# Optimization experiments

Hardware: AMD Instinct MI355X
Metric: run time of the kernel (lower is better)

The kernel has to match this reference:

```python
import jax, jax.numpy as jnp
import numpy as np

N, E, F_IN, EDGE_DIM, EMB, H, L, DENSE = 50000, 800000, 16, 4, 32, 4, 2, 128
HC = EMB * H


def setup_inputs() -> dict:
    ks = iter(jax.random.split(jax.random.key(0), 64))

    def w(shape, fan):
        return jax.random.normal(next(ks), shape, jnp.float32) / np.float32(np.sqrt(fan))

    inp = {}
    inp['x'] = jax.random.normal(next(ks), (N, F_IN), jnp.float32)
    inp['edge_index'] = jax.random.randint(next(ks), (2, E), 0, N, jnp.int32)
    inp['edge_attr'] = jax.random.normal(next(ks), (E, EDGE_DIM), jnp.float32)
    # layer-0 TransformerConv (F_IN -> EMB, H heads) + transf Linear
    inp['Wq0'] = w((F_IN, HC), F_IN); inp['bq0'] = w((HC,), HC)
    inp['Wk0'] = w((F_IN, HC), F_IN); inp['bk0'] = w((HC,), HC)
    inp['Wv0'] = w((F_IN, HC), F_IN); inp['bv0'] = w((HC,), HC)
    inp['We0'] = w((EDGE_DIM, HC), EDGE_DIM)
    inp['Ws0'] = w((F_IN, HC), F_IN); inp['bs0'] = w((HC,), HC)
    inp['Wt0'] = w((HC, EMB), HC); inp['bt0'] = w((EMB,), EMB)
    # stacked L inner layers (EMB -> EMB)
    inp['Wq'] = w((L, EMB, HC), EMB); inp['bq'] = w((L, HC), HC)
    inp['Wk'] = w((L, EMB, HC), EMB); inp['bk'] = w((L, HC), HC)
    inp['Wv'] = w((L, EMB, HC), EMB); inp['bv'] = w((L, HC), HC)
    inp['We'] = w((L, EDGE_DIM, HC), EDGE_DIM)
    inp['Ws'] = w((L, EMB, HC), EMB); inp['bs'] = w((L, HC), HC)
    inp['Wt'] = w((L, HC, EMB), HC); inp['bt'] = w((L, EMB), EMB)
    # dense head
    inp['W1'] = w((EMB, DENSE), EMB); inp['b1'] = w((DENSE,), DENSE)
    inp['W2'] = w((DENSE, DENSE // 2), DENSE); inp['b2'] = w((DENSE // 2,), DENSE)
    inp['W3'] = w((DENSE // 2, 1), DENSE // 2); inp['b3'] = w((1,), 1)
    return inp


def _tconv(h, edge_attr, src, dst, Wq, bq, Wk, bk, Wv, bv, We, Ws, bs):
    """PyG TransformerConv: edge-conditioned multi-head attention + root skip."""
    n = h.shape[0]
    q = (h @ Wq + bq).reshape(n, H, EMB)
    k = (h @ Wk + bk).reshape(n, H, EMB)
    v = (h @ Wv + bv).reshape(n, H, EMB)
    e = (edge_attr @ We).reshape(-1, H, EMB)          # [E,H,C]
    kj = k[src] + e                                   # gather + edge bias
    logits = (q[dst] * kj).sum(-1) / np.float32(np.sqrt(EMB))  # [E,H]
    m = jax.ops.segment_max(logits, dst, num_segments=n)       # segment softmax
    p = jnp.exp(logits - m[dst])
    z = jax.ops.segment_sum(p, dst, num_segments=n)
    alpha = p / (z[dst] + 1e-16)
    msg = (v[src] + e) * alpha[:, :, None]
    out = jax.ops.segment_sum(msg, dst, num_segments=n).reshape(n, HC)
    return out + h @ Ws + bs                          # root_weight skip


def _forward(x, edge_attr, Wq0, bq0, Wk0, bk0, Wv0, bv0, We0, Ws0, bs0, Wt0, bt0,
             Wq, bq, Wk, bk, Wv, bv, We, Ws, bs, Wt, bt,
             W1, b1, W2, b2, W3, b3, edge_index):
    src, dst = edge_index[0], edge_index[1]
    h = _tconv(x, edge_attr, src, dst, Wq0, bq0, Wk0, bk0, Wv0, bv0, We0, Ws0, bs0)
    h = jax.nn.relu(h @ Wt0 + bt0)
    for i in range(L):
        h = _tconv(h, edge_attr, src, dst, Wq[i], bq[i], Wk[i], bk[i],
                   Wv[i], bv[i], We[i], Ws[i], bs[i])
        h = jax.nn.relu(h @ Wt[i] + bt[i])
    h = jax.nn.relu(h @ W1 + b1)
    h = jax.nn.relu(h @ W2 + b2)
    return jax.nn.sigmoid(h @ W3 + b3)                # [N,1]


def reference(x, edge_index, edge_attr, Wq0, bq0, Wk0, bk0, Wv0, bv0, We0, Ws0, bs0,
              Wt0, bt0, Wq, bq, Wk, bk, Wv, bv, We, Ws, bs, Wt, bt,
              W1, b1, W2, b2, W3, b3):
    return _forward(x, edge_attr, Wq0, bq0, Wk0, bk0, Wv0, bv0, We0, Ws0, bs0,
                    Wt0, bt0, Wq, bq, Wk, bk, Wv, bv, We, Ws, bs, Wt, bt,
                    W1, b1, W2, b2, W3, b3, edge_index)
```

## Files before the change

### kernel.cpp

```cpp
#include <hip/hip_runtime.h>

#define NN 50000
#define EE 800000
#define FIN 16
#define EDIM 4
#define EMB 32
#define NH 4
#define HC 128
#define NL 2
#define DENSE 128
#define QNPB 50
#define SBLK 49

__device__ __forceinline__ float2 h2f2(unsigned int u) {
    union { unsigned int u; _Float16 h[2]; } c; c.u = u;
    return make_float2((float)c.h[0], (float)c.h[1]);
}
__device__ __forceinline__ unsigned int pkh2(float a, float b) {
    union { unsigned int u; _Float16 h[2]; } c;
    c.h[0] = (_Float16)a; c.h[1] = (_Float16)b; return c.u;
}

__global__ void hist_kernel(const int* __restrict__ dst, int* __restrict__ counts) {
    int e = blockIdx.x * blockDim.x + threadIdx.x;
    if (e < EE) atomicAdd(&counts[dst[e]], 1);
}

__global__ __launch_bounds__(1024) void scan1_kernel(const int* __restrict__ cursor,
                                                     int* __restrict__ row_ptr,
                                                     int* __restrict__ bsum) {
    __shared__ int wsum[16];
    __shared__ int wpre[17];
    int tid = threadIdx.x, lane = tid & 63, wid = tid >> 6;
    int i = blockIdx.x * 1024 + tid;
    int v = (i < NN) ? cursor[i] : 0;
    int incl = v;
    #pragma unroll
    for (int off = 1; off < 64; off <<= 1) {
        int t = __shfl_up(incl, off, 64);
        if (lane >= off) incl += t;
    }
    if (lane == 63) wsum[wid] = incl;
    __syncthreads();
    if (tid == 0) {
        int acc = 0;
        #pragma unroll
        for (int w = 0; w < 16; ++w) { wpre[w] = acc; acc += wsum[w]; }
        wpre[16] = acc;
    }
    __syncthreads();
    if (i < NN) row_ptr[i] = wpre[wid] + incl - v;
    if (tid == 0) bsum[blockIdx.x] = wpre[16];
}

__global__ __launch_bounds__(1024) void scan3_kernel(int* __restrict__ row_ptr,
                                                     int* __restrict__ cursor,
                                                     const int* __restrict__ bsum) {
    __shared__ int boff_s;
    __shared__ int total_s;
    int tid = threadIdx.x;
    if (tid < 64) {
        int v = (tid < SBLK) ? bsum[tid] : 0;
        int incl = v;
        #pragma unroll
        for (int off = 1; off < 64; off <<= 1) {
            int u = __shfl_up(incl, off, 64);
            if (tid >= off) incl += u;
        }
        if (tid == (int)blockIdx.x) boff_s = incl - v;
        if (tid == 63) total_s = incl;
    }
    __syncthreads();
    int i = blockIdx.x * 1024 + tid;
    if (i < NN) {
        int r = row_ptr[i] + boff_s;
        row_ptr[i] = r;
        cursor[i] = r;
    }
    if (blockIdx.x == 0 && tid == 0) row_ptr[NN] = total_s;
}

__global__ void scatter_kernel(const int* __restrict__ src, const int* __restrict__ dst,
                               const float* __restrict__ ea, int* __restrict__ cursor,
                               uint4* __restrict__ edges) {
    int e = blockIdx.x * blockDim.x + threadIdx.x;
    if (e >= EE) return;
    int d = dst[e];
    int pos = atomicAdd(&cursor[d], 1);
    float4 q = *reinterpret_cast<const float4*>(ea + (size_t)e * 4);
    uint4 rec;
    rec.x = (unsigned int)src[e];
    rec.y = pkh2(q.x, q.y);
    rec.z = pkh2(q.z, q.w);
    rec.w = 0u;
    edges[pos] = rec;
}

__global__ __launch_bounds__(512) void qkvs0_kernel(const float* __restrict__ x,
        const float* __restrict__ Wq, const float* __restrict__ bq,
        const float* __restrict__ Wk, const float* __restrict__ bk,
        const float* __restrict__ Wv, const float* __restrict__ bv,
        const float* __restrict__ Ws, const float* __restrict__ bs,
        _Float16* __restrict__ Qh, _Float16* __restrict__ kvh,
        float* __restrict__ Out) {
    __shared__ __align__(16) float hs[QNPB * FIN];
    int tid = threadIdx.x;
    int m = tid >> 7, c = tid & 127;
    const float* W; const float* b;
    switch (m) {
        case 0:  W = Wq; b = bq; break;
        case 1:  W = Wk; b = bk; break;
        case 2:  W = Wv; b = bv; break;
        default: W = Ws; b = bs; break;
    }
    float w[FIN];
    #pragma unroll
    for (int f = 0; f < FIN; ++f) w[f] = W[f * HC + c];
    float bias = b[c];
    int node0 = blockIdx.x * QNPB;
    {
        const float4* src4 = (const float4*)(x + (size_t)node0 * FIN);
        float4* dst4 = (float4*)hs;
        for (int i = tid; i < QNPB * FIN / 4; i += 512) dst4[i] = src4[i];
    }
    __syncthreads();
    const float4* hs4 = (const float4*)hs;
    for (int k = 0; k < QNPB; ++k) {
        float s = bias;
        #pragma unroll
        for (int f4 = 0; f4 < FIN / 4; ++f4) {
            float4 hv = hs4[k * (FIN / 4) + f4];
            s += hv.x * w[4 * f4] + hv.y * w[4 * f4 + 1]
               + hv.z * w[4 * f4 + 2] + hv.w * w[4 * f4 + 3];
        }
        size_t n = node0 + k;
        if      (m == 0) Qh[n * HC + c] = (_Float16)s;
        else if (m == 1) kvh[n * 256 + 2 * c] = (_Float16)s;
        else if (m == 2) kvh[n * 256 + 2 * c + 1] = (_Float16)s;
        else             Out[n * HC + c] = s;
    }
}

__global__ __launch_bounds__(512) void ftq_kernel(const float* __restrict__ Wt,
        const float* __restrict__ bt,
        const float* __restrict__ Wq, const float* __restrict__ bq,
        const float* __restrict__ Wk, const float* __restrict__ bk,
        const float* __restrict__ Wv, const float* __restrict__ bv,
        const float* __restrict__ Ws, const float* __restrict__ bs,
        _Float16* __restrict__ Qh, _Float16* __restrict__ kvh,
        float* __restrict__ Out) {
    __shared__ __align__(16) float os[QNPB * HC];
    __shared__ __align__(16) float hs[QNPB * EMB];
    int tid = threadIdx.x;
    int node0 = blockIdx.x * QNPB;
    int g = tid >> 7;

    {
        const float4* src4 = (const float4*)(Out + (size_t)node0 * HC);
        float4* dst4 = (float4*)os;
        for (int i = tid; i < QNPB * HC / 4; i += 512) dst4[i] = src4[i];
    }

    int cT = (tid & 127) >> 2, seg = tid & 3;
    float wt[32];
    #pragma unroll
    for (int j = 0; j < 32; ++j) wt[j] = Wt[(seg * 32 + j) * EMB + cT];
    float btc = bt[cT];
    __syncthreads();
    for (int k = g; k < QNPB; k += 4) {
        float p = 0.f;
        const float4* r4 = (const float4*)(os + k * HC + seg * 32);
        #pragma unroll
        for (int j4 = 0; j4 < 8; ++j4) {
            float4 rv = r4[j4];
            p += rv.x * wt[4 * j4] + rv.y * wt[4 * j4 + 1]
               + rv.z * wt[4 * j4 + 2] + rv.w * wt[4 * j4 + 3];
        }
        p += __shfl_xor(p, 1, 64);
        p += __shfl_xor(p, 2, 64);
        if (seg == 0) hs[k * EMB + cT] = fmaxf(p + btc, 0.f);
    }
    __syncthreads();

    int m = tid >> 7, c = tid & 127;
    const float* W; const float* b;
    switch (m) {
        case 0:  W = Wq; b = bq; break;
        case 1:  W = Wk; b = bk; break;
        case 2:  W = Wv; b = bv; break;
        default: W = Ws; b = bs; break;
    }
    float w[EMB];
    #pragma unroll
    for (int f = 0; f < EMB; ++f) w[f] = W[f * HC + c];
    float bias = b[c];
    const float4* hs4 = (const float4*)hs;
    for (int k = 0; k < QNPB; ++k) {
        float s = bias;
        #pragma unroll
        for (int f4 = 0; f4 < EMB / 4; ++f4) {
            float4 hv = hs4[k * (EMB / 4) + f4];
            s += hv.x * w[4 * f4] + hv.y * w[4 * f4 + 1]
               + hv.z * w[4 * f4 + 2] + hv.w * w[4 * f4 + 3];
        }
        size_t n = node0 + k;
        if      (m == 0) Qh[n * HC + c] = (_Float16)s;
        else if (m == 1) kvh[n * 256 + 2 * c] = (_Float16)s;
        else if (m == 2) kvh[n * 256 + 2 * c + 1] = (_Float16)s;
        else             Out[n * HC + c] = s;
    }
}

__global__ __launch_bounds__(256) void edge_attn_kernel(const int* __restrict__ row_ptr,
        const uint4* __restrict__ edges,
        const float* __restrict__ We,
        const _Float16* __restrict__ Qh, const uint2* __restrict__ kvp,
        float2* __restrict__ Out) {
    int n = blockIdx.x * 4 + (threadIdx.x >> 6);
    int lane = threadIdx.x & 63;
    int ch0 = 2 * lane, ch1 = 2 * lane + 1;
    float we0[4], we1[4];
    #pragma unroll
    for (int d = 0; d < 4; ++d) { we0[d] = We[d * HC + ch0]; we1[d] = We[d * HC + ch1]; }
    float2 q = h2f2(((const unsigned int*)Qh)[(size_t)n * 64 + lane]);
    int start = row_ptr[n], end = row_ptr[n + 1];
    float z = 0.f, acc0 = 0.f, acc1 = 0.f;
    const float SC = 0.17677669529663687f;
    int i = start;
    for (; i + 1 < end; i += 2) {
        uint4 rA = edges[i], rB = edges[i + 1];
        int sA = (int)rA.x, sB = (int)rB.x;
        sA = sA < 0 ? 0 : (sA >= NN ? NN - 1 : sA);
        sB = sB < 0 ? 0 : (sB >= NN ? NN - 1 : sB);
        uint2 kvA = kvp[(size_t)sA * 64 + lane];
        uint2 kvB = kvp[(size_t)sB * 64 + lane];
        float2 eAxy = h2f2(rA.y), eAzw = h2f2(rA.z);
        float2 eBxy = h2f2(rB.y), eBzw = h2f2(rB.z);
        float eA0 = eAxy.x * we0[0] + eAxy.y * we0[1] + eAzw.x * we0[2] + eAzw.y * we0[3];
        float eA1 = eAxy.x * we1[0] + eAxy.y * we1[1] + eAzw.x * we1[2] + eAzw.y * we1[3];
        float eB0 = eBxy.x * we0[0] + eBxy.y * we0[1] + eBzw.x * we0[2] + eBzw.y * we0[3];
        float eB1 = eBxy.x * we1[0] + eBxy.y * we1[1] + eBzw.x * we1[2] + eBzw.y * we1[3];
        float2 kvA0 = h2f2(kvA.x), kvA1 = h2f2(kvA.y);
        float2 kvB0 = h2f2(kvB.x), kvB1 = h2f2(kvB.y);
        float pA = q.x * (kvA0.x + eA0) + q.y * (kvA1.x + eA1);
        float pB = q.x * (kvB0.x + eB0) + q.y * (kvB1.x + eB1);
        #pragma unroll
        for (int off = 1; off < 16; off <<= 1) {
            pA += __shfl_xor(pA, off, 64);
            pB += __shfl_xor(pB, off, 64);
        }
        float xA = __expf(pA * SC), xB = __expf(pB * SC);
        z += xA + xB;
        acc0 += xA * (kvA0.y + eA0) + xB * (kvB0.y + eB0);
        acc1 += xA * (kvA1.y + eA1) + xB * (kvB1.y + eB1);
    }
    if (i < end) {
        uint4 r = edges[i];
        int s = (int)r.x;
        s = s < 0 ? 0 : (s >= NN ? NN - 1 : s);
        uint2 kv = kvp[(size_t)s * 64 + lane];
        float2 exy = h2f2(r.y), ezw = h2f2(r.z);
        float e0 = exy.x * we0[0] + exy.y * we0[1] + ezw.x * we0[2] + ezw.y * we0[3];
        float e1 = exy.x * we1[0] + exy.y * we1[1] + ezw.x * we1[2] + ezw.y * we1[3];
        float2 kv0 = h2f2(kv.x), kv1 = h2f2(kv.y);
        float p = q.x * (kv0.x + e0) + q.y * (kv1.x + e1);
        #pragma unroll
        for (int off = 1; off < 16; off <<= 1) p += __shfl_xor(p, off, 64);
        float x = __expf(p * SC);
        z += x;
        acc0 += x * (kv0.y + e0);
        acc1 += x * (kv1.y + e1);
    }
    float inv = 1.f / (z + 1e-16f);
    size_t oi = (size_t)n * 64 + lane;
    float2 o = Out[oi];
    o.x += acc0 * inv;
    o.y += acc1 * inv;
    Out[oi] = o;
}

__global__ __launch_bounds__(512) void head2_kernel(const float* __restrict__ Outb,
        const float* __restrict__ Wt, const float* __restrict__ bt,
        const float* __restrict__ W1, const float* __restrict__ b1,
        const float* __restrict__ W2, const float* __restrict__ b2,
        const float* __restrict__ W3, const float* __restrict__ b3,
        float* __restrict__ out) {
    __shared__ __align__(16) float os[QNPB * HC];
    __shared__ __align__(16) float hs[QNPB * EMB];
    __shared__ __align__(16) float d2s[QNPB * 64];
    float* d1s = os;
    int tid = threadIdx.x;
    int node0 = blockIdx.x * QNPB;
    int g = tid >> 7;

    {
        const float4* src4 = (const float4*)(Outb + (size_t)node0 * HC);
        float4* dst4 = (float4*)os;
        for (int i = tid; i < QNPB * HC / 4; i += 512) dst4[i] = src4[i];
    }

    int cT = (tid & 127) >> 2, seg = tid & 3;
    float wt[32];
    #pragma unroll
    for (int j = 0; j < 32; ++j) wt[j] = Wt[(seg * 32 + j) * EMB + cT];
    float btc = bt[cT];
    __syncthreads();
    for (int k = g; k < QNPB; k += 4) {
        float p = 0.f;
        const float4* r4 = (const float4*)(os + k * HC + seg * 32);
        #pragma unroll
        for (int j4 = 0; j4 < 8; ++j4) {
            float4 rv = r4[j4];
            p += rv.x * wt[4 * j4] + rv.y * wt[4 * j4 + 1]
               + rv.z * wt[4 * j4 + 2] + rv.w * wt[4 * j4 + 3];
        }
        p += __shfl_xor(p, 1, 64);
        p += __shfl_xor(p, 2, 64);
        if (seg == 0) hs[k * EMB + cT] = fmaxf(p + btc, 0.f);
    }
    __syncthreads();

    int c1 = tid & 127;
    float w1[32];
    #pragma unroll
    for (int f = 0; f < 32; ++f) w1[f] = W1[f * DENSE + c1];
    float b1c = b1[c1];
    const float4* hs4 = (const float4*)hs;
    for (int k = g; k < QNPB; k += 4) {
        float s = b1c;
        #pragma unroll
        for (int f4 = 0; f4 < 8; ++f4) {
            float4 hv = hs4[k * 8 + f4];
            s += hv.x * w1[4 * f4] + hv.y * w1[4 * f4 + 1]
               + hv.z * w1[4 * f4 + 2] + hv.w * w1[4 * f4 + 3];
        }
        d1s[k * DENSE + c1] = fmaxf(s, 0.f);
    }
    __syncthreads();

    int c2 = (tid & 127) >> 1, hh = tid & 1;
    float w2[64];
    #pragma unroll
    for (int j = 0; j < 64; ++j) w2[j] = W2[(hh * 64 + j) * 64 + c2];
    float b2c = b2[c2];
    for (int k = g; k < QNPB; k += 4) {
        float p = 0.f;
        const float4* r4 = (const float4*)(d1s + k * DENSE + hh * 64);
        #pragma unroll
        for (int j4 = 0; j4 < 16; ++j4) {
            float4 rv = r4[j4];
            p += rv.x * w2[4 * j4] + rv.y * w2[4 * j4 + 1]
               + rv.z * w2[4 * j4 + 2] + rv.w * w2[4 * j4 + 3];
        }
        p += __shfl_xor(p, 1, 64);
        if (hh == 0) d2s[k * 64 + c2] = fmaxf(p + b2c, 0.f);
    }
    __syncthreads();

    int w = tid >> 6, lane = tid & 63;
    float w3r = W3[lane];
    float b3r = b3[0];
    for (int k = w; k < QNPB; k += 8) {
        float t = d2s[k * 64 + lane] * w3r;
        #pragma unroll
        for (int off = 1; off < 64; off <<= 1) t += __shfl_xor(t, off, 64);
        if (lane == 0) out[node0 + k] = 1.f / (1.f + __expf(-(t + b3r)));
    }
}

extern "C" void kernel_launch(void* const* d_in, const int* in_sizes, int n_in,
                              void* d_out, int out_size, void* d_ws, size_t ws_size,
                              hipStream_t stream) {
    const float* x   = (const float*)d_in[0];
    const int*   ei  = (const int*)d_in[1];
    const float* ea  = (const float*)d_in[2];
    const float* Wq0 = (const float*)d_in[3];  const float* bq0 = (const float*)d_in[4];
    const float* Wk0 = (const float*)d_in[5];  const float* bk0 = (const float*)d_in[6];
    const float* Wv0 = (const float*)d_in[7];  const float* bv0 = (const float*)d_in[8];
    const float* We0 = (const float*)d_in[9];
    const float* Ws0 = (const float*)d_in[10]; const float* bs0 = (const float*)d_in[11];
    const float* Wt0 = (const float*)d_in[12]; const float* bt0 = (const float*)d_in[13];
    const float* WqL = (const float*)d_in[14]; const float* bqL = (const float*)d_in[15];
    const float* WkL = (const float*)d_in[16]; const float* bkL = (const float*)d_in[17];
    const float* WvL = (const float*)d_in[18]; const float* bvL = (const float*)d_in[19];
    const float* WeL = (const float*)d_in[20];
    const float* WsL = (const float*)d_in[21]; const float* bsL = (const float*)d_in[22];
    const float* WtL = (const float*)d_in[23]; const float* btL = (const float*)d_in[24];
    const float* W1  = (const float*)d_in[25]; const float* b1  = (const float*)d_in[26];
    const float* W2  = (const float*)d_in[27]; const float* b2  = (const float*)d_in[28];
    const float* W3  = (const float*)d_in[29]; const float* b3  = (const float*)d_in[30];
    float* out = (float*)d_out;

    char* ws = (char*)d_ws;
    size_t off = 0;
    auto alloc = [&](size_t bytes) -> void* {
        void* p = ws + off; off = (off + bytes + 255) & ~(size_t)255; return p;
    };
    int*      cursor  = (int*)     alloc((size_t)NN * 4);
    int*      row_ptr = (int*)     alloc((size_t)(NN + 1) * 4);
    int*      bsum    = (int*)     alloc((size_t)SBLK * 4);
    uint4*    edges   = (uint4*)   alloc((size_t)EE * 16);
    _Float16* Qh      = (_Float16*)alloc((size_t)NN * HC * 2);
    _Float16* kvh     = (_Float16*)alloc((size_t)NN * HC * 2 * 2);
    float*    Outb    = (float*)   alloc((size_t)NN * HC * 4);

    hipMemsetAsync(cursor, 0, (size_t)NN * 4, stream);
    hist_kernel<<<(EE + 255) / 256, 256, 0, stream>>>(ei + EE, cursor);
    scan1_kernel<<<SBLK, 1024, 0, stream>>>(cursor, row_ptr, bsum);
    scan3_kernel<<<SBLK, 1024, 0, stream>>>(row_ptr, cursor, bsum);
    scatter_kernel<<<(EE + 255) / 256, 256, 0, stream>>>(ei, ei + EE, ea, cursor, edges);

    const uint2* kvp = (const uint2*)kvh;
    float2* Out2 = (float2*)Outb;

    qkvs0_kernel<<<NN / QNPB, 512, 0, stream>>>(x, Wq0, bq0, Wk0, bk0, Wv0, bv0,
                                                Ws0, bs0, Qh, kvh, Outb);
    edge_attn_kernel<<<NN / 4, 256, 0, stream>>>(row_ptr, edges, We0, Qh, kvp, Out2);

    ftq_kernel<<<NN / QNPB, 512, 0, stream>>>(Wt0, bt0,
        WqL, bqL, WkL, bkL, WvL, bvL, WsL, bsL, Qh, kvh, Outb);
    edge_attn_kernel<<<NN / 4, 256, 0, stream>>>(row_ptr, edges, WeL, Qh, kvp, Out2);

    ftq_kernel<<<NN / QNPB, 512, 0, stream>>>(WtL, btL,
        WqL + EMB * HC, bqL + HC, WkL + EMB * HC, bkL + HC,
        WvL + EMB * HC, bvL + HC, WsL + EMB * HC, bsL + HC, Qh, kvh, Outb);
    edge_attn_kernel<<<NN / 4, 256, 0, stream>>>(row_ptr, edges,
        WeL + EDIM * HC, Qh, kvp, Out2);

    head2_kernel<<<NN / QNPB, 512, 0, stream>>>(Outb, WtL + (size_t)HC * EMB, btL + EMB,
                                                W1, b1, W2, b2, W3, b3, out);
}
```

Before: 621.6 us.

## Use packed fp16 dot products, interleave K/V layout, prefetch edges in attention

The edge attention loop now computes the edge-bias and q·k products with packed half-precision fdot2 instructions and adds K/V and the edge bias in packed fp16. The K/V interleave layout changes so each lane loads its two K and two V halves as adjacent pairs. Edge records for the next pair are prefetched with nontemporal loads one iteration ahead, and the source-index clamp is removed in favour of raw byte-offset addressing. The goal is fewer ALU conversions and instructions per edge and better latency hiding, at the cost of reduced accumulation precision and no bounds guard on source indices.

```diff
diff --git a/kernel.cpp b/kernel.cpp
--- a/kernel.cpp
+++ b/kernel.cpp
@@ -11,6 +11,25 @@
 #define DENSE 128
 #define QNPB 50
 #define SBLK 49
+
+typedef _Float16 h2 __attribute__((ext_vector_type(2)));
+typedef unsigned int u32x4 __attribute__((ext_vector_type(4)));
+union HU { unsigned int u; h2 h; };
+
+__device__ __forceinline__ h2 u2h(unsigned int u) { HU c; c.u = u; return c.h; }
+__device__ __forceinline__ unsigned int h2u(h2 h) { HU c; c.h = h; return c.u; }
+
+#if defined(__has_builtin)
+#  if __has_builtin(__builtin_amdgcn_fdot2)
+#    define FDOT2(a, b, c) __builtin_amdgcn_fdot2((a), (b), (c), false)
+#  endif
+#endif
+#ifndef FDOT2
+__device__ __forceinline__ float fdot2_sw(h2 a, h2 b, float c) {
+    return fmaf((float)a.x, (float)b.x, fmaf((float)a.y, (float)b.y, c));
+}
+#  define FDOT2(a, b, c) fdot2_sw((a), (b), (c))
+#endif
 
 __device__ __forceinline__ float2 h2f2(unsigned int u) {
     union { unsigned int u; _Float16 h[2]; } c; c.u = u;
@@ -125,6 +144,7 @@
     }
     __syncthreads();
     const float4* hs4 = (const float4*)hs;
+    int kvi = ((c >> 1) << 2) + (c & 1);
     for (int k = 0; k < QNPB; ++k) {
         float s = bias;
         #pragma unroll
@@ -135,8 +155,8 @@
         }
         size_t n = node0 + k;
         if      (m == 0) Qh[n * HC + c] = (_Float16)s;
-        else if (m == 1) kvh[n * 256 + 2 * c] = (_Float16)s;
-        else if (m == 2) kvh[n * 256 + 2 * c + 1] = (_Float16)s;
+        else if (m == 1) kvh[n * 256 + kvi] = (_Float16)s;
+        else if (m == 2) kvh[n * 256 + kvi + 2] = (_Float16)s;
         else             Out[n * HC + c] = s;
     }
 }
@@ -195,6 +215,7 @@
     for (int f = 0; f < EMB; ++f) w[f] = W[f * HC + c];
     float bias = b[c];
     const float4* hs4 = (const float4*)hs;
+    int kvi = ((c >> 1) << 2) + (c & 1);
     for (int k = 0; k < QNPB; ++k) {
         float s = bias;
         #pragma unroll
@@ -205,8 +226,8 @@
         }
         size_t n = node0 + k;
         if      (m == 0) Qh[n * HC + c] = (_Float16)s;
-        else if (m == 1) kvh[n * 256 + 2 * c] = (_Float16)s;
-        else if (m == 2) kvh[n * 256 + 2 * c + 1] = (_Float16)s;
+        else if (m == 1) kvh[n * 256 + kvi] = (_Float16)s;
+        else if (m == 2) kvh[n * 256 + kvi + 2] = (_Float16)s;
         else             Out[n * HC + c] = s;
     }
 }
@@ -214,36 +235,48 @@
 __global__ __launch_bounds__(256) void edge_attn_kernel(const int* __restrict__ row_ptr,
         const uint4* __restrict__ edges,
         const float* __restrict__ We,
-        const _Float16* __restrict__ Qh, const uint2* __restrict__ kvp,
+        const unsigned int* __restrict__ Qp, const uint2* __restrict__ kvp,
         float2* __restrict__ Out) {
     int n = blockIdx.x * 4 + (threadIdx.x >> 6);
     int lane = threadIdx.x & 63;
-    int ch0 = 2 * lane, ch1 = 2 * lane + 1;
-    float we0[4], we1[4];
-    #pragma unroll
-    for (int d = 0; d < 4; ++d) { we0[d] = We[d * HC + ch0]; we1[d] = We[d * HC + ch1]; }
-    float2 q = h2f2(((const unsigned int*)Qh)[(size_t)n * 64 + lane]);
+    int c0 = 2 * lane, c1 = 2 * lane + 1;
+    const u32x4* ev = (const u32x4*)edges;
+    h2 w01_0 = { (_Float16)We[0 * HC + c0], (_Float16)We[1 * HC + c0] };
+    h2 w23_0 = { (_Float16)We[2 * HC + c0], (_Float16)We[3 * HC + c0] };
+    h2 w01_1 = { (_Float16)We[0 * HC + c1], (_Float16)We[1 * HC + c1] };
+    h2 w23_1 = { (_Float16)We[2 * HC + c1], (_Float16)We[3 * HC + c1] };
+    h2 q = u2h(Qp[(size_t)n * 64 + lane]);
     int start = row_ptr[n], end = row_ptr[n + 1];
     float z = 0.f, acc0 = 0.f, acc1 = 0.f;
     const float SC = 0.17677669529663687f;
+    const char* kvb = (const char*)kvp;
+    unsigned int loff = (unsigned int)lane << 3;
     int i = start;
-    for (; i + 1 < end; i += 2) {
-        uint4 rA = edges[i], rB = edges[i + 1];
-        int sA = (int)rA.x, sB = (int)rB.x;
-        sA = sA < 0 ? 0 : (sA >= NN ? NN - 1 : sA);
-        sB = sB < 0 ? 0 : (sB >= NN ? NN - 1 : sB);
-        uint2 kvA = kvp[(size_t)sA * 64 + lane];
-        uint2 kvB = kvp[(size_t)sB * 64 + lane];
-        float2 eAxy = h2f2(rA.y), eAzw = h2f2(rA.z);
-        float2 eBxy = h2f2(rB.y), eBzw = h2f2(rB.z);
-        float eA0 = eAxy.x * we0[0] + eAxy.y * we0[1] + eAzw.x * we0[2] + eAzw.y * we0[3];
-        float eA1 = eAxy.x * we1[0] + eAxy.y * we1[1] + eAzw.x * we1[2] + eAzw.y * we1[3];
-        float eB0 = eBxy.x * we0[0] + eBxy.y * we0[1] + eBzw.x * we0[2] + eBzw.y * we0[3];
-        float eB1 = eBxy.x * we1[0] + eBxy.y * we1[1] + eBzw.x * we1[2] + eBzw.y * we1[3];
-        float2 kvA0 = h2f2(kvA.x), kvA1 = h2f2(kvA.y);
-        float2 kvB0 = h2f2(kvB.x), kvB1 = h2f2(kvB.y);
-        float pA = q.x * (kvA0.x + eA0) + q.y * (kvA1.x + eA1);
-        float pB = q.x * (kvB0.x + eB0) + q.y * (kvB1.x + eB1);
+    u32x4 rA, rB;
+    if (i + 1 < end) {
+        rA = __builtin_nontemporal_load(ev + i);
+        rB = __builtin_nontemporal_load(ev + i + 1);
+    }
+    while (i + 1 < end) {
+        uint2 kvA = *(const uint2*)(kvb + ((rA[0] << 9) + loff));
+        uint2 kvB = *(const uint2*)(kvb + ((rB[0] << 9) + loff));
+        int inext = i + 2;
+        int p0 = inext, p1 = inext + 1;
+        if (p1 >= end) { p0 = i; p1 = i; }
+        u32x4 rA2 = __builtin_nontemporal_load(ev + p0);
+        u32x4 rB2 = __builtin_nontemporal_load(ev + p1);
+        h2 eaA01 = u2h(rA[1]), eaA23 = u2h(rA[2]);
+        h2 eaB01 = u2h(rB[1]), eaB23 = u2h(rB[2]);
+        float eA0 = FDOT2(eaA01, w01_0, FDOT2(eaA23, w23_0, 0.f));
+        float eA1 = FDOT2(eaA01, w01_1, FDOT2(eaA23, w23_1, 0.f));
+        float eB0 = FDOT2(eaB01, w01_0, FDOT2(eaB23, w23_0, 0.f));
+        float eB1 = FDOT2(eaB01, w01_1, FDOT2(eaB23, w23_1, 0.f));
+        h2 eApk = { (_Float16)eA0, (_Float16)eA1 };
+        h2 eBpk = { (_Float16)eB0, (_Float16)eB1 };
+        h2 kA = u2h(kvA.x), vA = u2h(kvA.y);
+        h2 kB = u2h(kvB.x), vB = u2h(kvB.y);
+        float pA = FDOT2(q, kA + eApk, 0.f);
+        float pB = FDOT2(q, kB + eBpk, 0.f);
         #pragma unroll
         for (int off = 1; off < 16; off <<= 1) {
             pA += __shfl_xor(pA, off, 64);
@@ -251,25 +284,29 @@
         }
         float xA = __expf(pA * SC), xB = __expf(pB * SC);
         z += xA + xB;
-        acc0 += xA * (kvA0.y + eA0) + xB * (kvB0.y + eB0);
-        acc1 += xA * (kvA1.y + eA1) + xB * (kvB1.y + eB1);
+        h2 veA = vA + eApk, veB = vB + eBpk;
+        float2 vfA = h2f2(h2u(veA)), vfB = h2f2(h2u(veB));
+        acc0 += xA * vfA.x + xB * vfB.x;
+        acc1 += xA * vfA.y + xB * vfB.y;
+        rA = rA2; rB = rB2; i = inext;
     }
     if (i < end) {
-        uint4 r = edges[i];
-        int s = (int)r.x;
-        s = s < 0 ? 0 : (s >= NN ? NN - 1 : s);
-        uint2 kv = kvp[(size_t)s * 64 + lane];
-        float2 exy = h2f2(r.y), ezw = h2f2(r.z);
-        float e0 = exy.x * we0[0] + exy.y * we0[1] + ezw.x * we0[2] + ezw.y * we0[3];
-        float e1 = exy.x * we1[0] + exy.y * we1[1] + ezw.x * we1[2] + ezw.y * we1[3];
-        float2 kv0 = h2f2(kv.x), kv1 = h2f2(kv.y);
-        float p = q.x * (kv0.x + e0) + q.y * (kv1.x + e1);
+        u32x4 r = __builtin_nontemporal_load(ev + i);
+        uint2 kv = *(const uint2*)(kvb + ((r[0] << 9) + loff));
+        h2 ea01 = u2h(r[1]), ea23 = u2h(r[2]);
+        float e0 = FDOT2(ea01, w01_0, FDOT2(ea23, w23_0, 0.f));
+        float e1 = FDOT2(ea01, w01_1, FDOT2(ea23, w23_1, 0.f));
+        h2 epk = { (_Float16)e0, (_Float16)e1 };
+        h2 k = u2h(kv.x), v = u2h(kv.y);
+        float p = FDOT2(q, k + epk, 0.f);
         #pragma unroll
         for (int off = 1; off < 16; off <<= 1) p += __shfl_xor(p, off, 64);
         float x = __expf(p * SC);
         z += x;
-        acc0 += x * (kv0.y + e0);
-        acc1 += x * (kv1.y + e1);
+        h2 ve = v + epk;
+        float2 vf = h2f2(h2u(ve));
+        acc0 += x * vf.x;
+        acc1 += x * vf.y;
     }
     float inv = 1.f / (z + 1e-16f);
     size_t oi = (size_t)n * 64 + lane;
@@ -411,21 +448,22 @@
     scatter_kernel<<<(EE + 255) / 256, 256, 0, stream>>>(ei, ei + EE, ea, cursor, edges);
 
     const uint2* kvp = (const uint2*)kvh;
+    const unsigned int* Qp = (const unsigned int*)Qh;
     float2* Out2 = (float2*)Outb;
 
     qkvs0_kernel<<<NN / QNPB, 512, 0, stream>>>(x, Wq0, bq0, Wk0, bk0, Wv0, bv0,
                                                 Ws0, bs0, Qh, kvh, Outb);
-    edge_attn_kernel<<<NN / 4, 256, 0, stream>>>(row_ptr, edges, We0, Qh, kvp, Out2);
+    edge_attn_kernel<<<NN / 4, 256, 0, stream>>>(row_ptr, edges, We0, Qp, kvp, Out2);
 
     ftq_kernel<<<NN / QNPB, 512, 0, stream>>>(Wt0, bt0,
         WqL, bqL, WkL, bkL, WvL, bvL, WsL, bsL, Qh, kvh, Outb);
-    edge_attn_kernel<<<NN / 4, 256, 0, stream>>>(row_ptr, edges, WeL, Qh, kvp, Out2);
+    edge_attn_kernel<<<NN / 4, 256, 0, stream>>>(row_ptr, edges, WeL, Qp, kvp, Out2);
 
     ftq_kernel<<<NN / QNPB, 512, 0, stream>>>(WtL, btL,
         WqL + EMB * HC, bqL + HC, WkL + EMB * HC, bkL + HC,
         WvL + EMB * HC, bvL + HC, WsL + EMB * HC, bsL + HC, Qh, kvh, Outb);
     edge_attn_kernel<<<NN / 4, 256, 0, stream>>>(row_ptr, edges,
-        WeL + EDIM * HC, Qh, kvp, Out2);
+        WeL + EDIM * HC, Qp, kvp, Out2);
 
     head2_kernel<<<NN / QNPB, 512, 0, stream>>>(Outb, WtL + (size_t)HC * EMB, btL + EMB,
                                                 W1, b1, W2, b2, W3, b3, out);
```

Result: slower. 676.0 us (+8.7%).
